# Performance work log

Measured on AMD Instinct MI355X. Metric: run time of the kernel, lower is better.

The kernel has to match this reference:

```python
import jax, jax.numpy as jnp
import numpy as np
from jax import lax

N = 512            # in_channel == out_channel
TOKENS = (16, 2048)


def _pair_order(n):
    # Reck-mesh rotation order: outer loop over pivot row i, inner loop j = n-1 .. i+1.
    ps, qs = [], []
    for i in range(n):
        for j in range(n - 1, i, -1):
            ps.append(i)
            qs.append(j)
    return np.asarray(ps, np.int32), np.asarray(qs, np.int32)


def _reconstruct(delta, phi):
    # Rebuild an n x n orthogonal matrix from n(n-1)/2 Givens angles (phi) and
    # a diagonal sign/scale vector (delta): U = diag(delta) @ R_last @ ... @ R_first,
    # where each R(p,q,phi) rotates rows p,q. Faithful sequential recurrence via lax.scan.
    n = delta.shape[0]
    ps, qs = _pair_order(n)
    c, s = jnp.cos(phi), jnp.sin(phi)

    def step(U, xs):
        p, q, ck, sk = xs
        rp = U[p]  # dynamic row gather
        rq = U[q]
        U = U.at[p].set(ck * rp - sk * rq)
        U = U.at[q].set(sk * rp + ck * rq)
        return U, None

    U0 = jnp.eye(n, dtype=delta.dtype)
    U, _ = lax.scan(step, U0, (jnp.asarray(ps), jnp.asarray(qs), c, s))
    return delta[:, None] * U


def setup_inputs() -> dict:
    key = jax.random.key(0)
    ks = jax.random.split(key, 6)
    npairs = N * (N - 1) // 2
    return {
        "x": jax.random.normal(ks[0], (*TOKENS, N), jnp.float32),
        "phi_U": jax.random.normal(ks[1], (npairs,), jnp.float32),
        "delta_U": jax.random.normal(ks[2], (N,), jnp.float32),
        "phi_V": jax.random.normal(ks[3], (npairs,), jnp.float32),
        "delta_V": jax.random.normal(ks[4], (N,), jnp.float32),
        "sigma": jax.random.normal(ks[5], (N,), jnp.float32),
    }


def reference(x, phi_U, delta_U, phi_V, delta_V, sigma):
    U = _reconstruct(delta_U, phi_U)          # [out, out]
    V = _reconstruct(delta_V, phi_V)          # [in, in]
    W = U @ (sigma[:, None] * V)              # U @ diag(sigma) @ V  (square case)
    return x @ W.T                            # F.linear(x, W), no bias
```

## Files before the change

kernel.cpp:

```cpp
#include <hip/hip_runtime.h>
#include <cmath>


#define NDIM 512
#define NPAIR 130816
#define MAT (NDIM * NDIM)

__device__ __forceinline__ int T_of(int i) { return (i * (1023 - i)) >> 1; }

__device__ __forceinline__ int pivot_of(int k) {
    int lo = 0, hi = 511;
    while (lo < hi) {
        int mid = (lo + hi + 1) >> 1;
        if (T_of(mid) <= k) lo = mid; else hi = mid - 1;
    }
    return lo;
}

__global__ __launch_bounds__(256) void trig_kernel(const float* __restrict__ pU,
                                                   const float* __restrict__ pV,
                                                   float2* __restrict__ csU,
                                                   float2* __restrict__ csV) {
    int idx = blockIdx.x * 256 + threadIdx.x;
    if (idx < NPAIR) {
        float s, c;
        sincosf(pU[idx], &s, &c);
        csU[idx] = make_float2(c, s);
    } else if (idx < 2 * NPAIR) {
        int m = idx - NPAIR;
        float s, c;
        sincosf(pV[m], &s, &c);
        csV[m] = make_float2(c, s);
    }
}

__global__ __launch_bounds__(64) void group_kernel(const float2* __restrict__ csU,
                                                   const float2* __restrict__ csV,
                                                   float* __restrict__ bufA,
                                                   int R, int capA) {
    __shared__ float v[NDIM * 32];
    const int lane = threadIdx.x;
    if (lane >= 32) return;
    const int col0 = blockIdx.x * 32;
    const int col  = col0 + lane;
    const int g    = blockIdx.y;
    const int side = blockIdx.z;
    const int k0 = g * R, k1 = k0 + R;
    const int i0 = pivot_of(k0);
    float* out = bufA + ((size_t)(side * capA + g)) * MAT;

    if (col0 + 32 <= i0) {
        for (int r = 0; r < NDIM; ++r)
            out[(size_t)r * NDIM + col] = (r == col) ? 1.f : 0.f;
        return;
    }
    const float2* __restrict__ csp = side ? csV : csU;

    for (int r = 0; r < NDIM; ++r)
        v[r * 32 + lane] = (r == col) ? 1.f : 0.f;

    int i = i0;
    int j = 511 - (k0 - T_of(i0));
    int k = k0;
    while (k < k1 && i < 511) {
        float vi = v[i * 32 + lane];
        int cnt = min(k1 - k, j - i);
        #pragma unroll 4
        for (int t = 0; t < cnt; ++t) {
            float2 cs = csp[k + t];
            float vj  = v[(j - t) * 32 + lane];
            float vjn = fmaf(cs.y, vi, cs.x * vj);
            vi        = fmaf(cs.x, vi, -(cs.y * vj));
            v[(j - t) * 32 + lane] = vjn;
        }
        k += cnt; j -= cnt;
        v[i * 32 + lane] = vi;
        if (j == i) { ++i; j = 511; }
    }
    for (int r = 0; r < NDIM; ++r)
        out[(size_t)r * NDIM + col] = v[r * 32 + lane];
}

__global__ __launch_bounds__(256) void combine_kernel(const float* __restrict__ src,
                                                      float* __restrict__ dst,
                                                      int srcCap, int dstCap,
                                                      int half, int R, int P) {
    const int side = blockIdx.z / P, m = blockIdx.z % P;
    const int bx = blockIdx.x & 7, by = blockIdx.x >> 3;
    const int row0 = by * 64, col0 = bx * 64;
    const float* __restrict__ X = src + ((size_t)(side * srcCap + 2 * m + 1)) * MAT;
    const float* __restrict__ Y = src + ((size_t)(side * srcCap + 2 * m)) * MAT;
    float* __restrict__ C = dst + ((size_t)(side * dstCap + m)) * MAT;
    const int ax = pivot_of((2 * m * half + half) * R);
    const int ay = pivot_of((2 * m * half) * R);
    const int tid = threadIdx.x;

    if (row0 + 64 <= ax) {
        for (int t = tid; t < 64 * 16; t += 256) {
            int r = t >> 4, q = (t & 15) * 4;
            size_t off = (size_t)(row0 + r) * NDIM + col0 + q;
            *(float4*)&C[off] = *(const float4*)&Y[off];
        }
        return;
    }
    if (col0 + 64 <= ay) {
        for (int t = tid; t < 64 * 16; t += 256) {
            int r = t >> 4, q = (t & 15) * 4;
            size_t off = (size_t)(row0 + r) * NDIM + col0 + q;
            *(float4*)&C[off] = *(const float4*)&X[off];
        }
        return;
    }

    __shared__ float Xs[64][36];
    __shared__ float Ys[32][68];
    const int tx = tid & 15, ty = tid >> 4;
    float acc[4][4] = {};
    const int kt0 = (row0 >= ax) ? (ax >> 5) : 0;
    for (int kt = kt0; kt < 16; ++kt) {
        {
            int r = tid >> 2, q = (tid & 3) * 4;
            const float* xr = X + (size_t)(row0 + r) * NDIM + kt * 32;
            *(float4*)&Xs[r][q]      = *(const float4*)(xr + q);
            *(float4*)&Xs[r][q + 16] = *(const float4*)(xr + q + 16);
        }
        {
            int kk = tid >> 4, cq = (tid & 15) * 4;
            *(float4*)&Ys[kk][cq]      = *(const float4*)(Y + (size_t)(kt * 32 + kk) * NDIM + col0 + cq);
            *(float4*)&Ys[kk + 16][cq] = *(const float4*)(Y + (size_t)(kt * 32 + kk + 16) * NDIM + col0 + cq);
        }
        __syncthreads();
        #pragma unroll
        for (int kk = 0; kk < 32; ++kk) {
            float av[4] = {Xs[ty * 4 + 0][kk], Xs[ty * 4 + 1][kk],
                           Xs[ty * 4 + 2][kk], Xs[ty * 4 + 3][kk]};
            float4 B = *(const float4*)&Ys[kk][tx * 4];
            float bv[4] = {B.x, B.y, B.z, B.w};
            #pragma unroll
            for (int mm = 0; mm < 4; ++mm)
                #pragma unroll
                for (int nn = 0; nn < 4; ++nn)
                    acc[mm][nn] = fmaf(av[mm], bv[nn], acc[mm][nn]);
        }
        __syncthreads();
    }
    #pragma unroll
    for (int mm = 0; mm < 4; ++mm) {
        float4 st = make_float4(acc[mm][0], acc[mm][1], acc[mm][2], acc[mm][3]);
        *(float4*)&C[(size_t)(row0 + ty * 4 + mm) * NDIM + col0 + tx * 4] = st;
    }
}

__global__ __launch_bounds__(256) void wasm_kernel(const float* __restrict__ Ru,
                                                   const float* __restrict__ Rv,
                                                   const float* __restrict__ dU,
                                                   const float* __restrict__ dV,
                                                   const float* __restrict__ sg,
                                                   float* __restrict__ W) {
    const int bx = blockIdx.x & 7, by = blockIdx.x >> 3;
    const int row0 = by * 64, col0 = bx * 64;
    __shared__ float Xs[64][36];
    __shared__ float Ys[32][68];
    const int tid = threadIdx.x;
    const int tx = tid & 15, ty = tid >> 4;
    float acc[4][4] = {};
    for (int kt = 0; kt < 16; ++kt) {
        {
            int r = tid >> 2, q = (tid & 3) * 4;
            const float* xr = Ru + (size_t)(row0 + r) * NDIM + kt * 32;
            *(float4*)&Xs[r][q]      = *(const float4*)(xr + q);
            *(float4*)&Xs[r][q + 16] = *(const float4*)(xr + q + 16);
        }
        {
            int kk = tid >> 4, cq = (tid & 15) * 4;
            int kg = kt * 32 + kk;
            float sd = sg[kg] * dV[kg];
            float4 b = *(const float4*)(Rv + (size_t)kg * NDIM + col0 + cq);
            b.x *= sd; b.y *= sd; b.z *= sd; b.w *= sd;
            *(float4*)&Ys[kk][cq] = b;
            int kg2 = kg + 16;
            float sd2 = sg[kg2] * dV[kg2];
            float4 b2 = *(const float4*)(Rv + (size_t)kg2 * NDIM + col0 + cq);
            b2.x *= sd2; b2.y *= sd2; b2.z *= sd2; b2.w *= sd2;
            *(float4*)&Ys[kk + 16][cq] = b2;
        }
        __syncthreads();
        #pragma unroll
        for (int kk = 0; kk < 32; ++kk) {
            float av[4] = {Xs[ty * 4 + 0][kk], Xs[ty * 4 + 1][kk],
                           Xs[ty * 4 + 2][kk], Xs[ty * 4 + 3][kk]};
            float4 B = *(const float4*)&Ys[kk][tx * 4];
            float bv[4] = {B.x, B.y, B.z, B.w};
            #pragma unroll
            for (int mm = 0; mm < 4; ++mm)
                #pragma unroll
                for (int nn = 0; nn < 4; ++nn)
                    acc[mm][nn] = fmaf(av[mm], bv[nn], acc[mm][nn]);
        }
        __syncthreads();
    }
    #pragma unroll
    for (int mm = 0; mm < 4; ++mm) {
        float du = dU[row0 + ty * 4 + mm];
        float4 st = make_float4(acc[mm][0] * du, acc[mm][1] * du,
                                acc[mm][2] * du, acc[mm][3] * du);
        *(float4*)&W[(size_t)(row0 + ty * 4 + mm) * NDIM + col0 + tx * 4] = st;
    }
}

__global__ __launch_bounds__(256) void gemm_kernel(const float* __restrict__ x,
                                                   const float* __restrict__ W,
                                                   float* __restrict__ out) {
    const int col0 = blockIdx.x * 64;
    const int row0 = blockIdx.y * 128;
    __shared__ float Xs[32][132];
    __shared__ float Ys[32][68];
    const int tid = threadIdx.x;
    const int tx = tid & 15, ty = tid >> 4;
    float acc[8][4] = {};
    for (int kt = 0; kt < 16; ++kt) {
        {
            int r = tid & 127;
            int ks = (tid >> 7) * 16;
            const float* xr = x + (size_t)(row0 + r) * NDIM + kt * 32 + ks;
            #pragma unroll
            for (int u = 0; u < 4; ++u) {
                float4 vv = *(const float4*)(xr + u * 4);
                Xs[ks + u * 4 + 0][r] = vv.x;
                Xs[ks + u * 4 + 1][r] = vv.y;
                Xs[ks + u * 4 + 2][r] = vv.z;
                Xs[ks + u * 4 + 3][r] = vv.w;
            }
        }
        {
            int o = tid & 63;
            int ks = (tid >> 6) * 4;
            const float* wr = W + (size_t)(col0 + o) * NDIM + kt * 32;
            float4 w0 = *(const float4*)(wr + ks);
            float4 w1 = *(const float4*)(wr + ks + 16);
            Ys[ks + 0][o] = w0.x; Ys[ks + 1][o] = w0.y;
            Ys[ks + 2][o] = w0.z; Ys[ks + 3][o] = w0.w;
            Ys[ks + 16][o] = w1.x; Ys[ks + 17][o] = w1.y;
            Ys[ks + 18][o] = w1.z; Ys[ks + 19][o] = w1.w;
        }
        __syncthreads();
        #pragma unroll
        for (int kk = 0; kk < 32; ++kk) {
            float4 A0 = *(const float4*)&Xs[kk][ty * 8];
            float4 A1 = *(const float4*)&Xs[kk][ty * 8 + 4];
            float4 B  = *(const float4*)&Ys[kk][tx * 4];
            float av[8] = {A0.x, A0.y, A0.z, A0.w, A1.x, A1.y, A1.z, A1.w};
            float bv[4] = {B.x, B.y, B.z, B.w};
            #pragma unroll
            for (int mm = 0; mm < 8; ++mm)
                #pragma unroll
                for (int nn = 0; nn < 4; ++nn)
                    acc[mm][nn] = fmaf(av[mm], bv[nn], acc[mm][nn]);
        }
        __syncthreads();
    }
    #pragma unroll
    for (int mm = 0; mm < 8; ++mm) {
        float4 st = make_float4(acc[mm][0], acc[mm][1], acc[mm][2], acc[mm][3]);
        *(float4*)&out[(size_t)(row0 + ty * 8 + mm) * NDIM + col0 + tx * 4] = st;
    }
}

extern "C" void kernel_launch(void* const* d_in, const int* in_sizes, int n_in,
                              void* d_out, int out_size, void* d_ws, size_t ws_size,
                              hipStream_t stream) {
    (void)in_sizes; (void)n_in; (void)out_size;
    const float* xp   = (const float*)d_in[0];
    const float* phiU = (const float*)d_in[1];
    const float* dUp  = (const float*)d_in[2];
    const float* phiV = (const float*)d_in[3];
    const float* dVp  = (const float*)d_in[4];
    const float* sgp  = (const float*)d_in[5];
    float* out = (float*)d_out;
    float* wsf = (float*)d_ws;

    int G = 16;
    while (G > 1) {
        size_t needFloats = (size_t)4 * NPAIR + (size_t)2 * G * MAT
                          + (size_t)G * MAT + MAT;
        if (needFloats * 4 <= ws_size) break;
        G >>= 1;
    }
    const int R = NPAIR / G;

    float2* csU = (float2*)wsf;
    float2* csV = csU + NPAIR;
    float* bufA = wsf + (size_t)4 * NPAIR;
    float* bufB = bufA + (size_t)2 * G * MAT;
    const int capB = (G > 1) ? G / 2 : 1;
    float* Wbuf = (G > 1) ? (bufB + (size_t)2 * capB * MAT) : bufB;

    trig_kernel<<<dim3((2 * NPAIR + 255) / 256), 256, 0, stream>>>(phiU, phiV, csU, csV);

    group_kernel<<<dim3(16, G, 2), 64, 0, stream>>>(csU, csV, bufA, R, G);

    const float* cur = bufA;
    float* oth = bufB;
    int curCap = G, othCap = capB;
    for (int P = G / 2, half = 1; P >= 1; P >>= 1, half <<= 1) {
        combine_kernel<<<dim3(64, 1, 2 * P), 256, 0, stream>>>(cur, oth, curCap, othCap, half, R, P);
        const float* t = cur; cur = oth; oth = (float*)t;
        int tc = curCap; curCap = othCap; othCap = tc;
    }
    const float* Ru = cur;
    const float* Rv = cur + (size_t)curCap * MAT;

    wasm_kernel<<<dim3(64), 256, 0, stream>>>(Ru, Rv, dUp, dVp, sgp, Wbuf);

    gemm_kernel<<<dim3(8, 256), 256, 0, stream>>>(xp, Wbuf, out);
}
```

Before: 873.8 us.

## Software-pipeline Givens rotation chain with double-buffered row and angle prefetch

The sequential rotation loop in group_kernel now runs in batches of 8 rotations. It prefetches the next batch's shared-memory rows and cos/sin pairs into registers while computing the current batch, with pivot-boundary transitions encoded as per-step flags. Prefetching is limited to rotations before pivot 496, so every pivot run is long enough that a prefetched row is never one still pending a write. The goal is to hide LDS and global load latency in a latency-bound serial recurrence. The cost is higher register use and extra select logic per step; the remaining rotations fall back to the old loop, which no longer has its unroll pragma.

```diff
diff --git a/kernel.cpp b/kernel.cpp
--- a/kernel.cpp
+++ b/kernel.cpp
@@ -34,6 +34,35 @@
     }
 }
 
+
+#define GK_LOAD(R_, C_, S_, W_, B_)                                   \
+    {                                                                 \
+        _Pragma("unroll")                                             \
+        for (int u = 0; u < 8; ++u) {                                 \
+            int bnd = (pj == pi + 1);                                 \
+            R_[u] = v[pj * 32 + lane];                                \
+            float2 cs2 = csp[kp + u];                                 \
+            C_[u] = cs2.x; S_[u] = cs2.y;                             \
+            W_[u] = bnd ? pi : pj;                                    \
+            B_[u] = bnd;                                              \
+            pi += bnd;                                                \
+            pj = bnd ? 511 : (pj - 1);                                \
+        }                                                             \
+        kp += 8;                                                      \
+    }
+
+#define GK_COMP(R_, C_, S_, W_, B_)                                   \
+    {                                                                 \
+        _Pragma("unroll")                                             \
+        for (int u = 0; u < 8; ++u) {                                 \
+            float vj  = R_[u];                                        \
+            float vjn = fmaf(S_[u], vi, C_[u] * vj);                  \
+            float vin = fmaf(C_[u], vi, -(S_[u] * vj));               \
+            v[W_[u] * 32 + lane] = B_[u] ? vin : vjn;                 \
+            vi = B_[u] ? vjn : vin;                                   \
+        }                                                             \
+    }
+
 __global__ __launch_bounds__(64) void group_kernel(const float2* __restrict__ csU,
                                                    const float2* __restrict__ csV,
                                                    float* __restrict__ bufA,
@@ -62,10 +91,29 @@
     int i = i0;
     int j = 511 - (k0 - T_of(i0));
     int k = k0;
+
+    const int kSafe = T_of(496);
+    const int kEnd = (k1 < kSafe) ? k1 : kSafe;
+    const int nb = (kEnd > k) ? (kEnd - k) / 8 : 0;
+    if (nb > 0) {
+        float vi = v[i * 32 + lane];
+        int pi = i, pj = j, kp = k;
+        float rA[8], rB[8], cA[8], sA[8], cB[8], sB[8];
+        int wA[8], wB[8], bA[8], bB[8];
+        GK_LOAD(rA, cA, sA, wA, bA);
+        for (int b = 1; b < nb; ++b) {
+            if (b & 1) { GK_LOAD(rB, cB, sB, wB, bB); GK_COMP(rA, cA, sA, wA, bA); }
+            else       { GK_LOAD(rA, cA, sA, wA, bA); GK_COMP(rB, cB, sB, wB, bB); }
+        }
+        if (nb & 1) { GK_COMP(rA, cA, sA, wA, bA); }
+        else        { GK_COMP(rB, cB, sB, wB, bB); }
+        k = kp; i = pi; j = pj;
+        v[i * 32 + lane] = vi;
+    }
+
     while (k < k1 && i < 511) {
         float vi = v[i * 32 + lane];
         int cnt = min(k1 - k, j - i);
-        #pragma unroll 4
         for (int t = 0; t < cnt; ++t) {
             float2 cs = csp[k + t];
             float vj  = v[(j - t) * 32 + lane];
@@ -77,6 +125,7 @@
         v[i * 32 + lane] = vi;
         if (j == i) { ++i; j = 511; }
     }
+
     for (int r = 0; r < NDIM; ++r)
         out[(size_t)r * NDIM + col] = v[r * 32 + lane];
 }
```

Measured after the change: 1.384 ms. +58.4%, slower.

## Pad rotation coefficients and process Givens rotations in 32-row register blocks

Applied to the files above, without the earlier changes.

The trig kernel now writes cos/sin pairs into a padded layout, aligned per pivot row, with identity rotations filling the padding. This lets the group kernel process each pivot row in 32-row blocks. Coefficients are staged in shared memory, and each block's matrix values and coefficients are loaded into registers as float4/float2 vectors. The transposed per-lane shared layout with stride 514 is meant to allow vectorised LDS access and to cut the per-rotation global loads and LDS round trips. The costs are higher register pressure, extra padded rotations, and masking logic at block edges.

```diff
diff --git a/kernel.cpp b/kernel.cpp
--- a/kernel.cpp
+++ b/kernel.cpp
@@ -5,8 +5,16 @@
 #define NDIM 512
 #define NPAIR 130816
 #define MAT (NDIM * NDIM)
+#define VSTRIDE 514
+#define PCAP 131584
+#define PSLACK 520
+#define PTOT (PCAP + PSLACK)
 
 __device__ __forceinline__ int T_of(int i) { return (i * (1023 - i)) >> 1; }
+
+__device__ __forceinline__ int base_of(int i) {
+    return T_of(i) + 6 * (i >> 2) + ((0x6310 >> ((i & 3) * 4)) & 0xF);
+}
 
 __device__ __forceinline__ int pivot_of(int k) {
     int lo = 0, hi = 511;
@@ -22,23 +30,43 @@
                                                    float2* __restrict__ csU,
                                                    float2* __restrict__ csV) {
     int idx = blockIdx.x * 256 + threadIdx.x;
-    if (idx < NPAIR) {
-        float s, c;
-        sincosf(pU[idx], &s, &c);
-        csU[idx] = make_float2(c, s);
-    } else if (idx < 2 * NPAIR) {
-        int m = idx - NPAIR;
-        float s, c;
-        sincosf(pV[m], &s, &c);
-        csV[m] = make_float2(c, s);
-    }
-}
+    if (idx >= 2 * PTOT) return;
+    const int side = idx >= PTOT;
+    const int s = idx - side * PTOT;
+    const float* __restrict__ phi = side ? pV : pU;
+    float2* __restrict__ dst = side ? csV : csU;
+    int lo = 0, hi = 510;
+    while (lo < hi) {
+        int mid = (lo + hi + 1) >> 1;
+        if (base_of(mid) <= s) lo = mid; else hi = mid - 1;
+    }
+    const int i = lo, t = s - base_of(i), L = 511 - i;
+    float2 cs = make_float2(1.f, 0.f);
+    if (t < L) {
+        float sn, cn;
+        sincosf(phi[T_of(i) + t], &sn, &cn);
+        cs = make_float2(cn, sn);
+    }
+    dst[s] = cs;
+}
+
+#define DR(WREF, CC, SS) { const float vj_ = (WREF); const float cx_ = (CC), sx_ = (SS); \
+    (WREF) = fmaf(sx_, vi, cx_ * vj_); vi = fmaf(cx_, vi, -(sx_ * vj_)); }
+
+#define R2(A) \
+    DR(w2[15-(A)].y, c4[(A)].x, c4[(A)].y) \
+    DR(w2[15-(A)].x, c4[(A)].z, c4[(A)].w)
+
+#define GP(A) { \
+    { const int rr = rb31 - 2*(A);     if (rr < rLo || rr > rHi) { c4[(A)].x = 1.f; c4[(A)].y = 0.f; } } \
+    { const int rr = rb31 - 2*(A) - 1; if (rr < rLo || rr > rHi) { c4[(A)].z = 1.f; c4[(A)].w = 0.f; } } }
 
 __global__ __launch_bounds__(64) void group_kernel(const float2* __restrict__ csU,
                                                    const float2* __restrict__ csV,
                                                    float* __restrict__ bufA,
                                                    int R, int capA) {
-    __shared__ float v[NDIM * 32];
+    __shared__ float vs[32 * VSTRIDE];
+    __shared__ float2 csl[512];
     const int lane = threadIdx.x;
     if (lane >= 32) return;
     const int col0 = blockIdx.x * 32;
@@ -47,6 +75,7 @@
     const int side = blockIdx.z;
     const int k0 = g * R, k1 = k0 + R;
     const int i0 = pivot_of(k0);
+    const int e0 = k0 - T_of(i0);
     float* out = bufA + ((size_t)(side * capA + g)) * MAT;
 
     if (col0 + 32 <= i0) {
@@ -54,31 +83,65 @@
             out[(size_t)r * NDIM + col] = (r == col) ? 1.f : 0.f;
         return;
     }
-    const float2* __restrict__ csp = side ? csV : csU;
+    const float2* __restrict__ pcs = side ? csV : csU;
+    const int vb = lane * VSTRIDE;
+
+    {
+        const float2 z2 = make_float2(0.f, 0.f);
+        for (int r = 0; r < NDIM; r += 2)
+            *(float2*)&vs[vb + r] = z2;
+        vs[vb + col] = 1.f;
+    }
+
+    int i = i0, k = k0;
+    while (k < k1 && i < 511) {
+        const int L = 511 - i;
+        const int tStart = (i == i0) ? e0 : 0;
+        const int tEnd = min(L, tStart + (k1 - k));
+        const int rHi = 511 - tStart;
+        const int rLo = 512 - tEnd;
+        const int bHi = rHi >> 5, bLo = rLo >> 5;
+        const int sBase = 480 - 32 * bHi;
+        const int sCount = 32 * (bHi - bLo + 1);
+
+        {
+            const float2* __restrict__ src = pcs + base_of(i) + sBase;
+            #pragma unroll 4
+            for (int t = lane; t < sCount; t += 32)
+                csl[t] = src[t];
+        }
+
+        float vi = vs[vb + i];
+        for (int b = bHi; b >= bLo; --b) {
+            const int sT = 480 - 32 * b - sBase;
+            const int rb31 = 32 * b + 31;
+            float4 c4[16];
+            float2 w2[16];
+            #pragma unroll
+            for (int m = 0; m < 16; ++m)
+                c4[m] = *(const float4*)&csl[sT + 2 * m];
+            #pragma unroll
+            for (int m = 0; m < 16; ++m)
+                w2[m] = *(const float2*)&vs[vb + 32 * b + 2 * m];
+
+            if (32 * b < rLo || rb31 > rHi) {
+                GP(0)  GP(1)  GP(2)  GP(3)  GP(4)  GP(5)  GP(6)  GP(7)
+                GP(8)  GP(9)  GP(10) GP(11) GP(12) GP(13) GP(14) GP(15)
+            }
+            R2(0)  R2(1)  R2(2)  R2(3)  R2(4)  R2(5)  R2(6)  R2(7)
+            R2(8)  R2(9)  R2(10) R2(11) R2(12) R2(13) R2(14) R2(15)
+
+            #pragma unroll
+            for (int m = 0; m < 16; ++m)
+                *(float2*)&vs[vb + 32 * b + 2 * m] = w2[m];
+        }
+        vs[vb + i] = vi;
+        k += tEnd - tStart;
+        ++i;
+    }
 
     for (int r = 0; r < NDIM; ++r)
-        v[r * 32 + lane] = (r == col) ? 1.f : 0.f;
-
-    int i = i0;
-    int j = 511 - (k0 - T_of(i0));
-    int k = k0;
-    while (k < k1 && i < 511) {
-        float vi = v[i * 32 + lane];
-        int cnt = min(k1 - k, j - i);
-        #pragma unroll 4
-        for (int t = 0; t < cnt; ++t) {
-            float2 cs = csp[k + t];
-            float vj  = v[(j - t) * 32 + lane];
-            float vjn = fmaf(cs.y, vi, cs.x * vj);
-            vi        = fmaf(cs.x, vi, -(cs.y * vj));
-            v[(j - t) * 32 + lane] = vjn;
-        }
-        k += cnt; j -= cnt;
-        v[i * 32 + lane] = vi;
-        if (j == i) { ++i; j = 511; }
-    }
-    for (int r = 0; r < NDIM; ++r)
-        out[(size_t)r * NDIM + col] = v[r * 32 + lane];
+        out[(size_t)r * NDIM + col] = vs[vb + r];
 }
 
 __global__ __launch_bounds__(256) void combine_kernel(const float* __restrict__ src,
@@ -281,7 +344,7 @@
 
     int G = 16;
     while (G > 1) {
-        size_t needFloats = (size_t)4 * NPAIR + (size_t)2 * G * MAT
+        size_t needFloats = (size_t)4 * PTOT + (size_t)2 * G * MAT
                           + (size_t)G * MAT + MAT;
         if (needFloats * 4 <= ws_size) break;
         G >>= 1;
@@ -289,13 +352,13 @@
     const int R = NPAIR / G;
 
     float2* csU = (float2*)wsf;
-    float2* csV = csU + NPAIR;
-    float* bufA = wsf + (size_t)4 * NPAIR;
+    float2* csV = csU + PTOT;
+    float* bufA = wsf + (size_t)4 * PTOT;
     float* bufB = bufA + (size_t)2 * G * MAT;
     const int capB = (G > 1) ? G / 2 : 1;
     float* Wbuf = (G > 1) ? (bufB + (size_t)2 * capB * MAT) : bufB;
 
-    trig_kernel<<<dim3((2 * NPAIR + 255) / 256), 256, 0, stream>>>(phiU, phiV, csU, csV);
+    trig_kernel<<<dim3((2 * PTOT + 255) / 256), 256, 0, stream>>>(phiU, phiV, csU, csV);
 
     group_kernel<<<dim3(16, G, 2), 64, 0, stream>>>(csU, csV, bufA, R, G);
 
```

After: 814.2 us. 6.8% less time.
